# Performance work log

Measured on AMD Instinct MI355X. Metric: run time of the kernel, lower is better.

## Reference

```python
import jax, jax.numpy as jnp
import numpy as np
from functools import partial

NUM_ITERS = 3
NUM_CAPS = 8      # primary capsule count
NUM_CLASSES = 10
OUT_CH = 16       # digit capsule dim
INPUT_SIZE = 32 * 6 * 6  # 1152 primary capsule units per capsule map


def squash(s, axis=-1):
    # faithful to non_linear_squashing: s * (||s||^2/(1+||s||^2)) / (||s||+1e-10)
    norm_sqr = jnp.sum(s * s, axis=axis, keepdims=True)
    scale = jnp.sqrt(norm_sqr) + 1e-10
    mag = norm_sqr / (1.0 + norm_sqr)
    return s * mag / scale


def conv2d(x, w, b, stride):
    y = jax.lax.conv_general_dilated(
        x, w, window_strides=(stride, stride), padding='VALID',
        dimension_numbers=('NCHW', 'OIHW', 'NCHW'))
    return y + b[None, :, None, None]


def setup_inputs() -> dict:
    key = jax.random.key(0)
    ks = jax.random.split(key, 6)
    B = 256
    x = jax.random.normal(ks[0], (B, 1, 28, 28), dtype=jnp.float32)
    conv_w = jax.random.normal(ks[1], (256, 1, 9, 9), dtype=jnp.float32) * 0.05
    conv_b = jax.random.normal(ks[2], (256,), dtype=jnp.float32) * 0.05
    # 8 primary capsule conv units (256->32 each) fused into one 256->256 conv
    prim_w = jax.random.normal(ks[3], (NUM_CAPS * 32, 256, 9, 9), dtype=jnp.float32) * 0.02
    prim_b = jax.random.normal(ks[4], (NUM_CAPS * 32,), dtype=jnp.float32) * 0.02
    # digit routing weights (input_size, num_classes, out_channels, num_capsules)
    digit_w = jax.random.normal(ks[5], (INPUT_SIZE, NUM_CLASSES, OUT_CH, NUM_CAPS), dtype=jnp.float32)
    return {'x': x, 'conv_w': conv_w, 'conv_b': conv_b,
            'prim_w': prim_w, 'prim_b': prim_b, 'digit_w': digit_w}


def reference(x, conv_w, conv_b, prim_w, prim_b, digit_w):
    B = x.shape[0]
    # conv stack: 1->256 k9 s1 + ReLU  (28 -> 20); pool is MaxPool2d(1,1) = identity
    h = jax.nn.relu(conv2d(x, conv_w, conv_b, stride=1))  # (B,256,20,20)
    # primary capsules: 8 convs 256->32 k9 s2, no activation (nl_activation=False)
    p = conv2d(h, prim_w, prim_b, stride=2)               # (B,256,6,6)
    u = p.reshape(B, NUM_CAPS, -1)                        # (B,8,1152)
    u = squash(u, axis=-1)
    # digit layer with dynamic routing
    # u_i: (B, IS, 8);  u_j_i[b,i,c,o] = sum_k W[i,c,o,k] * u_i[b,i,k]
    u_i = jnp.transpose(u, (0, 2, 1))                     # (B,1152,8)
    u_j_i = jnp.einsum('icok,bik->bico', digit_w, u_i)    # (B,1152,10,16)
    b_ij = jnp.zeros((INPUT_SIZE, NUM_CLASSES), dtype=x.dtype)
    out = None
    for _ in range(NUM_ITERS):
        c_ij = jax.nn.softmax(b_ij, axis=0)               # softmax over input capsules (dim=1 in torch)
        s_j = jnp.einsum('ic,bico->bco', c_ij, u_j_i)     # (B,10,16)
        # original squashes (B,1,C,16,1) along dim=2 == the CLASS axis
        out = squash(s_j, axis=1)                         # (B,10,16)
        # agreement: mean over batch of <u_j_i, v_j>
        u_v = jnp.einsum('bico,bco->ic', u_j_i, out) / B  # (1152,10)
        b_ij = b_ij + u_v
    # torch returns out.squeeze(1) with shape (B, C, 16, 1)
    return out[..., None]
```

## Files before the change

### kernel.cpp

```cpp
#include <hip/hip_runtime.h>
#include <cstdint>
#include <cstddef>


typedef __attribute__((ext_vector_type(8))) short short8;
typedef __attribute__((ext_vector_type(4))) float f32x4;

#define PHALF 2359296

__device__ __forceinline__ unsigned short f2bf_rn(float x) {
    unsigned u = __float_as_uint(x);
    unsigned r = (u + 0x7fffu + ((u >> 16) & 1u)) >> 16;
    return (unsigned short)r;
}

__global__ void k_prep(const float* __restrict__ w2, const float* __restrict__ cw,
                       const float* __restrict__ dw,
                       unsigned short* __restrict__ wt,
                       unsigned short* __restrict__ wb1,
                       float* __restrict__ dwT2) {
    __shared__ float lw[20736];
    int blk = blockIdx.x, t = threadIdx.x;
    if (blk < 256) {
        int ocg = blk >> 3, icg = blk & 7;
        for (int idx = t; idx < 20736; idx += 256) {
            int row = idx / 81, k = idx % 81;
            int oc_l = row >> 5, ic_l = row & 31;
            lw[idx] = w2[((size_t)(ocg * 8 + oc_l) * 256 + icg * 32 + ic_l) * 81 + k];
        }
        __syncthreads();
        for (int idx = t; idx < 2592; idx += 256) {
            int k = idx >> 5;
            int r = idx & 31;
            int oc_l = r >> 2, sl = r & 3;
            unsigned short hi8[8];
            #pragma unroll
            for (int j = 0; j < 8; j++)
                hi8[j] = f2bf_rn(lw[(oc_l * 32 + sl * 8 + j) * 81 + k]);
            size_t o = ((size_t)(k * 256 + ocg * 8 + oc_l)) * 256 + icg * 32 + sl * 8;
            *(uint4*)&wt[o] = *(uint4*)hi8;
        }
    } else if (blk == 256) {
        for (int idx = t; idx < 24576; idx += 256) {
            int j = idx & 7, lane = (idx >> 3) & 63;
            int q = (idx >> 9) % 3, nt = idx / 1536;
            int oc = nt * 16 + (lane & 15);
            int kg = q * 32 + (lane >> 4) * 8 + j;
            float v = (kg < 81) ? cw[oc * 81 + kg] : 0.f;
            wb1[idx] = f2bf_rn(v);
        }
    } else {
        int co = blk - 257;
        int c = co >> 4, o = co & 15;
        const float* base = dw + c * 128 + o * 8;
        float* out = dwT2 + (size_t)co * 9216;
        for (int idx = t; idx < 9216; idx += 256) {
            int i = idx >> 3, k = idx & 7;
            out[idx] = base[(size_t)i * 1280 + k];
        }
    }
}

__global__ __launch_bounds__(256) void k_conv1m(
    const float* __restrict__ x, const unsigned short* __restrict__ wb1,
    const float* __restrict__ cb, unsigned short* __restrict__ h)
{
    __shared__ unsigned short xb[900];
    int b = blockIdx.x, ng = blockIdx.y, t = threadIdx.x;
    int w = t >> 6, l = t & 63;
    for (int idx = t; idx < 900; idx += 256) {
        int row = idx / 30, col = idx % 30;
        float v = (row < 28 && col < 28) ? x[(size_t)b * 784 + row * 28 + col] : 0.f;
        xb[idx] = f2bf_rn(v);
    }
    __syncthreads();
    int lane16 = l & 15, l4 = l >> 4;
    int ntile = (w == 0) ? 7 : 6;
    short8 afr[7][3];
    for (int i = 0; i < 7; i++) {
        if (i < ntile) {
            int mt = w + 4 * i;
            int pix = mt * 16 + lane16;
            int py = pix / 20, px = pix % 20;
            #pragma unroll
            for (int qq = 0; qq < 3; qq++) {
                int kbase = qq * 32 + l4 * 8;
                unsigned short tmp[8];
                int ky = kbase / 9, kx = kbase - 9 * (kbase / 9);
                #pragma unroll
                for (int j = 0; j < 8; j++) {
                    tmp[j] = xb[(py + ky) * 30 + px + kx];
                    kx++; if (kx == 9) { kx = 0; ky++; }
                }
                afr[i][qq] = *(short8*)tmp;
            }
        }
    }
    for (int nt0 = 0; nt0 < 8; nt0++) {
        int nt = ng * 8 + nt0;
        short8 bfr[3];
        #pragma unroll
        for (int qq = 0; qq < 3; qq++)
            bfr[qq] = *(const short8*)&wb1[(nt * 3 + qq) * 512 + l * 8];
        float bias = cb[nt * 16 + lane16];
        f32x4 acc[7] = {};
        for (int i = 0; i < 7; i++) {
            if (i < ntile) {
                #pragma unroll
                for (int qq = 0; qq < 3; qq++)
                    acc[i] = __builtin_amdgcn_mfma_f32_16x16x32_bf16(afr[i][qq], bfr[qq], acc[i], 0, 0, 0);
            }
        }
        for (int i = 0; i < 7; i++) {
            if (i < ntile) {
                int mt = w + 4 * i;
                int pixb = mt * 16 + l4 * 4;
                size_t base = ((size_t)b * 400 + pixb) * 256 + nt * 16 + lane16;
                #pragma unroll
                for (int r = 0; r < 4; r++) {
                    float v = fmaxf(acc[i][r] + bias, 0.f);
                    h[base + (size_t)r * 256] = f2bf_rn(v);
                }
            }
        }
    }
}

__global__ __launch_bounds__(256) void k_conv2m(
    const unsigned short* __restrict__ h,
    const unsigned short* __restrict__ wt,
    float* __restrict__ pp)
{
    __shared__ unsigned short smem[24576];
    const int t = threadIdx.x;
    const int w = t >> 6, l = t & 63;
    const int mb = blockIdx.x, nb = blockIdx.y, z = blockIdx.z;

    const unsigned short* src;
    int nld, sbase;
    unsigned rowbase[16];
    if (w < 2) {
        src = h; nld = 16; sbase = w * 8192;
        #pragma unroll
        for (int ld = 0; ld < 16; ld++) {
            int row = ld * 8 + (l >> 3);
            int c = l & 7;
            int g = c ^ (row & 7);
            int P = mb * 128 + row;
            int b = P / 36, o = P % 36;
            int oy = o / 6, ox = o % 6;
            rowbase[ld] = (unsigned)((b * 400 + oy * 40 + ox * 2) * 256 + z * 128 + w * 64 + g * 8);
        }
    } else {
        int hh = w - 2;
        src = wt; nld = 8; sbase = 16384 + hh * 4096;
        #pragma unroll
        for (int ld = 0; ld < 8; ld++) {
            int oc = ld * 8 + (l >> 3);
            int c = l & 7;
            int g = c ^ (oc & 7);
            rowbase[ld] = (unsigned)((nb * 64 + oc) * 256 + z * 128 + hh * 64 + g * 8);
        }
    }

    const int wm = w & 1, wn = w >> 1;
    const int lane16 = l & 15, q = l >> 4;

    f32x4 acc[4][2] = {};

    for (int ky = 0; ky < 9; ky++) {
        for (int kx = 0; kx < 9; kx++) {
            const unsigned kofs = (w < 2) ? (unsigned)((ky * 20 + kx) * 256)
                                          : (unsigned)((ky * 9 + kx) * 65536);
            __syncthreads();
            for (int ld = 0; ld < nld; ld++) {
                __builtin_amdgcn_global_load_lds(
                    (const __attribute__((address_space(1))) unsigned int*)(const void*)(src + rowbase[ld] + kofs),
                    (__attribute__((address_space(3))) unsigned int*)(void*)(smem + sbase + ld * 512),
                    16, 0, 0);
            }
            __syncthreads();
            #pragma unroll
            for (int hh = 0; hh < 2; hh++) {
                #pragma unroll
                for (int ic2 = 0; ic2 < 2; ic2++) {
                    short8 a[4], b[2];
                    #pragma unroll
                    for (int mt = 0; mt < 4; mt++) {
                        int pixL = wm * 64 + mt * 16 + lane16;
                        int ps = (ic2 * 4 + q) ^ (pixL & 7);
                        a[mt] = *(const short8*)(smem + hh * 8192 + pixL * 64 + ps * 8);
                    }
                    #pragma unroll
                    for (int nt = 0; nt < 2; nt++) {
                        int ocL = wn * 32 + nt * 16 + lane16;
                        int ps = (ic2 * 4 + q) ^ (ocL & 7);
                        b[nt] = *(const short8*)(smem + 16384 + hh * 4096 + ocL * 64 + ps * 8);
                    }
                    #pragma unroll
                    for (int mt = 0; mt < 4; mt++)
                        #pragma unroll
                        for (int nt = 0; nt < 2; nt++)
                            acc[mt][nt] = __builtin_amdgcn_mfma_f32_16x16x32_bf16(a[mt], b[nt], acc[mt][nt], 0, 0, 0);
                }
            }
        }
    }

    float* pout = pp + (size_t)z * PHALF;
    #pragma unroll
    for (int mt = 0; mt < 4; mt++) {
        int pixG = mb * 128 + wm * 64 + mt * 16 + q * 4;
        int b = pixG / 36, p36 = pixG % 36;
        #pragma unroll
        for (int nt = 0; nt < 2; nt++) {
            int oc = nb * 64 + wn * 32 + nt * 16 + lane16;
            f32x4 v = acc[mt][nt];
            *(f32x4*)&pout[((size_t)(b * 256 + oc)) * 36 + p36] = v;
        }
    }
}

__global__ void k_squash1(const float* __restrict__ pp, const float* __restrict__ prim_b,
                          float* __restrict__ U) {
    __shared__ float red[4];
    int b = blockIdx.x >> 3, cap = blockIdx.x & 7;
    int t = threadIdx.x;
    const float* pa = pp + ((size_t)b * 256 + cap * 32) * 36;
    const float* pc = pa + PHALF;
    float v[5];
    float ss = 0.f;
    #pragma unroll
    for (int j = 0; j < 5; j++) {
        int idx = t + j * 256;
        if (idx < 1152) {
            int ch_l = idx / 36;
            float val = pa[idx] + pc[idx] + prim_b[cap * 32 + ch_l];
            v[j] = val; ss += val * val;
        } else v[j] = 0.f;
    }
    for (int off = 32; off; off >>= 1) ss += __shfl_down(ss, off);
    if ((t & 63) == 0) red[t >> 6] = ss;
    __syncthreads();
    float n2 = red[0] + red[1] + red[2] + red[3];
    float f = (n2 / (1.0f + n2)) / (sqrtf(n2) + 1e-10f);
    #pragma unroll
    for (int j = 0; j < 5; j++) {
        int idx = t + j * 256;
        if (idx < 1152) U[(size_t)b * 9216 + idx * 8 + cap] = v[j] * f;
    }
}

__global__ void k_ut(const float* __restrict__ U, float* __restrict__ UT) {
    __shared__ float tl[64][65];
    int ikb = blockIdx.x, bb = blockIdx.y, t = threadIdx.x;
    for (int idx = t; idx < 1024; idx += 256) {
        int row = idx >> 4, c4 = idx & 15;
        float4 v = *(const float4*)&U[(size_t)(bb * 64 + row) * 9216 + ikb * 64 + c4 * 4];
        tl[c4 * 4 + 0][row] = v.x;
        tl[c4 * 4 + 1][row] = v.y;
        tl[c4 * 4 + 2][row] = v.z;
        tl[c4 * 4 + 3][row] = v.w;
    }
    __syncthreads();
    for (int idx = t; idx < 1024; idx += 256) {
        int row = idx >> 4, c4 = idx & 15;
        float4 v = make_float4(tl[row][c4 * 4 + 0], tl[row][c4 * 4 + 1],
                               tl[row][c4 * 4 + 2], tl[row][c4 * 4 + 3]);
        *(float4*)&UT[(size_t)(ikb * 64 + row) * 256 + bb * 64 + c4 * 4] = v;
    }
}

__global__ __launch_bounds__(256) void k_gemm1(const float* __restrict__ U,
                                               const float* __restrict__ dwT2,
                                               const float* __restrict__ bij,
                                               float* __restrict__ part,
                                               int uniform) {
    __shared__ float Us[32 * 36];
    __shared__ float WsT[5120];
    __shared__ float cl[360];
    __shared__ float red[256];
    __shared__ float cmx[10], cinv[10];
    int mb = blockIdx.x, kc = blockIdx.y, t = threadIdx.x;
    int tc = t & 15, tb = t >> 4;

    if (!uniform) {
        int c = t % 10, g = t / 10;
        float lmx = -1e30f;
        if (t < 250)
            for (int i = g; i < 1152; i += 25) lmx = fmaxf(lmx, bij[i * 10 + c]);
        red[t] = lmx;
        __syncthreads();
        if (t < 10) {
            float m = -1e30f;
            #pragma unroll
            for (int g2 = 0; g2 < 25; g2++) m = fmaxf(m, red[g2 * 10 + t]);
            cmx[t] = m;
        }
        __syncthreads();
        float lsum = 0.f;
        if (t < 250) {
            float m = cmx[c];
            for (int i = g; i < 1152; i += 25) lsum += expf(bij[i * 10 + c] - m);
        }
        red[t] = lsum;
        __syncthreads();
        if (t < 10) {
            float s2 = 0.f;
            #pragma unroll
            for (int g2 = 0; g2 < 25; g2++) s2 += red[g2 * 10 + t];
            cinv[t] = 1.0f / s2;
        }
        __syncthreads();
        for (int idx = t; idx < 360; idx += 256) {
            int i = kc * 36 + idx / 10, c2 = idx % 10;
            cl[idx] = expf(bij[i * 10 + c2] - cmx[c2]) * cinv[c2];
        }
    }

    const float uscale = 1.0f / 1152.0f;
    float acc[2][10] = {};
    for (int ks = 0; ks < 9; ks++) {
        __syncthreads();
        {
            int bb = t >> 3, k4 = t & 7;
            *(float4*)&Us[bb * 36 + k4 * 4] =
                *(const float4*)&U[(size_t)(mb * 32 + bb) * 9216 + kc * 288 + ks * 32 + k4 * 4];
        }
        #pragma unroll
        for (int pass = 0; pass < 5; pass++) {
            int s = t + pass * 256;
            int co = s >> 3, p = s & 7;
            int kq = p ^ (co & 7);
            int ikl = ks * 32 + kq * 4;
            float4 v = *(const float4*)&dwT2[(size_t)co * 9216 + kc * 288 + ikl];
            float sc = uniform ? uscale : cl[(ikl >> 3) * 10 + (co >> 4)];
            v.x *= sc; v.y *= sc; v.z *= sc; v.w *= sc;
            *(float4*)&WsT[s * 4] = v;
        }
        __syncthreads();
        float a0[32], a1[32];
        #pragma unroll
        for (int kq = 0; kq < 8; kq++) {
            float4 v0 = *(const float4*)&Us[(tb * 2) * 36 + kq * 4];
            float4 v1 = *(const float4*)&Us[(tb * 2 + 1) * 36 + kq * 4];
            a0[kq * 4 + 0] = v0.x; a0[kq * 4 + 1] = v0.y; a0[kq * 4 + 2] = v0.z; a0[kq * 4 + 3] = v0.w;
            a1[kq * 4 + 0] = v1.x; a1[kq * 4 + 1] = v1.y; a1[kq * 4 + 2] = v1.z; a1[kq * 4 + 3] = v1.w;
        }
        #pragma unroll
        for (int j = 0; j < 10; j++) {
            int co = tc + 16 * j;
            int cx = co & 7, cbase = co * 32;
            #pragma unroll
            for (int kq = 0; kq < 8; kq++) {
                float4 wv = *(const float4*)&WsT[cbase + ((kq ^ cx) << 2)];
                acc[0][j] += a0[kq * 4 + 0] * wv.x; acc[0][j] += a0[kq * 4 + 1] * wv.y;
                acc[0][j] += a0[kq * 4 + 2] * wv.z; acc[0][j] += a0[kq * 4 + 3] * wv.w;
                acc[1][j] += a1[kq * 4 + 0] * wv.x; acc[1][j] += a1[kq * 4 + 1] * wv.y;
                acc[1][j] += a1[kq * 4 + 2] * wv.z; acc[1][j] += a1[kq * 4 + 3] * wv.w;
            }
        }
    }
    #pragma unroll
    for (int r = 0; r < 2; r++)
        #pragma unroll
        for (int j = 0; j < 10; j++)
            part[(size_t)kc * 40960 + (mb * 32 + tb * 2 + r) * 160 + tc + 16 * j] = acc[r][j];
}

__global__ void k_redsq(const float* __restrict__ part, float* __restrict__ outT,
                        float* __restrict__ dout, int last) {
    __shared__ float sl[160];
    __shared__ float n2s[16];
    int b = blockIdx.x, t = threadIdx.x;
    float s = 0.f;
    if (t < 160) {
        for (int kc = 0; kc < 32; kc++) s += part[(size_t)kc * 40960 + b * 160 + t];
        sl[t] = s;
    }
    __syncthreads();
    if (t < 16) {
        float n2 = 0.f;
        #pragma unroll
        for (int c = 0; c < 10; c++) { float v = sl[c * 16 + t]; n2 += v * v; }
        n2s[t] = n2;
    }
    __syncthreads();
    if (t < 160) {
        float n2 = n2s[t & 15];
        float f = (n2 / (1.0f + n2)) / (sqrtf(n2) + 1e-10f);
        float r = s * f;
        if (last) dout[(size_t)b * 160 + t] = r;
        else      outT[(size_t)t * 256 + b] = r;
    }
}

__global__ __launch_bounds__(256) void k_g2uv(const float* __restrict__ UT,
                                              const float* __restrict__ outTg,
                                              const float* __restrict__ dw,
                                              float* __restrict__ bij, int init) {
    __shared__ float UsT[1024];
    __shared__ float OsT[5120];
    __shared__ float dwl[5120];
    __shared__ float sb[320];
    int blk = blockIdx.x, t = threadIdx.x;
    int tc = t & 15, tm = t >> 4;
    for (int idx = t; idx < 5120; idx += 256)
        dwl[idx] = dw[(size_t)blk * 5120 + idx];
    float acc[2][10] = {};
    for (int bs = 0; bs < 256; bs += 32) {
        __syncthreads();
        {
            int m = t >> 3, p = t & 7;
            int kq = p ^ (m & 7);
            *(float4*)&UsT[t * 4] =
                *(const float4*)&UT[(size_t)(blk * 32 + m) * 256 + bs + kq * 4];
        }
        #pragma unroll
        for (int pass = 0; pass < 5; pass++) {
            int s = t + pass * 256;
            int co = s >> 3, p = s & 7;
            int kq = p ^ (co & 7);
            *(float4*)&OsT[s * 4] =
                *(const float4*)&outTg[(size_t)co * 256 + bs + kq * 4];
        }
        __syncthreads();
        float a0[32], a1[32];
        int m0 = tm * 2, m1 = tm * 2 + 1;
        #pragma unroll
        for (int kq = 0; kq < 8; kq++) {
            float4 v0 = *(const float4*)&UsT[m0 * 32 + ((kq ^ (m0 & 7)) << 2)];
            float4 v1 = *(const float4*)&UsT[m1 * 32 + ((kq ^ (m1 & 7)) << 2)];
            a0[kq * 4 + 0] = v0.x; a0[kq * 4 + 1] = v0.y; a0[kq * 4 + 2] = v0.z; a0[kq * 4 + 3] = v0.w;
            a1[kq * 4 + 0] = v1.x; a1[kq * 4 + 1] = v1.y; a1[kq * 4 + 2] = v1.z; a1[kq * 4 + 3] = v1.w;
        }
        #pragma unroll
        for (int j = 0; j < 10; j++) {
            int co = tc + 16 * j;
            int cx = co & 7, cbase = co * 32;
            #pragma unroll
            for (int kq = 0; kq < 8; kq++) {
                float4 wv = *(const float4*)&OsT[cbase + ((kq ^ cx) << 2)];
                acc[0][j] += a0[kq * 4 + 0] * wv.x; acc[0][j] += a0[kq * 4 + 1] * wv.y;
                acc[0][j] += a0[kq * 4 + 2] * wv.z; acc[0][j] += a0[kq * 4 + 3] * wv.w;
                acc[1][j] += a1[kq * 4 + 0] * wv.x; acc[1][j] += a1[kq * 4 + 1] * wv.y;
                acc[1][j] += a1[kq * 4 + 2] * wv.z; acc[1][j] += a1[kq * 4 + 3] * wv.w;
            }
        }
    }
    #pragma unroll
    for (int r = 0; r < 2; r++) {
        int ik_l = tm * 2 + r;
        int i_l = ik_l >> 3, k = ik_l & 7;
        #pragma unroll
        for (int j = 0; j < 10; j++) {
            float v = acc[r][j] * dwl[i_l * 1280 + (j * 16 + tc) * 8 + k];
            v += __shfl_down(v, 8, 16);
            v += __shfl_down(v, 4, 16);
            v += __shfl_down(v, 2, 16);
            v += __shfl_down(v, 1, 16);
            if (tc == 0) sb[ik_l * 10 + j] = v;
        }
    }
    __syncthreads();
    if (t < 40) {
        int i_l = t / 10, c = t % 10;
        float s = 0.f;
        #pragma unroll
        for (int kk = 0; kk < 8; kk++) s += sb[(i_l * 8 + kk) * 10 + c];
        size_t o = (size_t)(blk * 4 + i_l) * 10 + c;
        float val = s * (1.0f / 256.0f);
        if (init) bij[o] = val;
        else      bij[o] += val;
    }
}

extern "C" void kernel_launch(void* const* d_in, const int* in_sizes, int n_in,
                              void* d_out, int out_size, void* d_ws, size_t ws_size,
                              hipStream_t stream) {
    const float* x      = (const float*)d_in[0];
    const float* conv_w = (const float*)d_in[1];
    const float* conv_b = (const float*)d_in[2];
    const float* prim_w = (const float*)d_in[3];
    const float* prim_b = (const float*)d_in[4];
    const float* dw     = (const float*)d_in[5];

    char* wsb = (char*)d_ws;
    unsigned short* h   = (unsigned short*)(wsb);
    unsigned short* wt  = (unsigned short*)(wsb + 52428800);
    float* pp   = (float*)(wsb + 63045632);
    float* U    = (float*)(wsb + 81920000);
    float* dwT2 = (float*)(wsb + 91357184);
    float* part = (float*)(wsb + 97255424);
    float* bij  = (float*)(wsb + 102544384);
    float* outT = (float*)(wsb + 102590464);
    float* UT   = (float*)(wsb + 102754304);
    unsigned short* wb1 = (unsigned short*)(wsb + 112191488);
    float* dout = (float*)d_out;

    k_prep<<<417, 256, 0, stream>>>(prim_w, conv_w, dw, wt, wb1, dwT2);
    k_conv1m<<<dim3(256, 2), 256, 0, stream>>>(x, wb1, conv_b, h);
    k_conv2m<<<dim3(72, 4, 2), 256, 0, stream>>>(h, wt, pp);
    k_squash1<<<2048, 256, 0, stream>>>(pp, prim_b, U);
    k_ut<<<dim3(144, 4), 256, 0, stream>>>(U, UT);

    k_gemm1<<<dim3(8, 32), 256, 0, stream>>>(U, dwT2, bij, part, 1);
    k_redsq<<<256, 256, 0, stream>>>(part, outT, dout, 0);
    k_g2uv<<<288, 256, 0, stream>>>(UT, outT, dw, bij, 1);
    k_gemm1<<<dim3(8, 32), 256, 0, stream>>>(U, dwT2, bij, part, 0);
    k_redsq<<<256, 256, 0, stream>>>(part, outT, dout, 0);
    k_g2uv<<<288, 256, 0, stream>>>(UT, outT, dw, bij, 0);
    k_gemm1<<<dim3(8, 32), 256, 0, stream>>>(U, dwT2, bij, part, 0);
    k_redsq<<<256, 256, 0, stream>>>(part, outT, dout, 1);
}
```

Before: 520.0 us.

## Fuse squash and routing iterations into one persistent kernel with grid barriers

Replaces ten separate launches (squash, transpose, three gemm/reduce/agreement rounds) with a single persistent kernel of 256 blocks that steps through the phases using a global atomic-counter barrier. It also drops the UT transpose by transposing U into shared memory inside the agreement phase. This is meant to remove kernel launch gaps and the extra transpose pass. In exchange it depends on all 256 blocks being co-resident, and the agreement phase over 288 units leaves blocks 32..255 idle while a few blocks do a second unit.

```diff
diff --git a/kernel.cpp b/kernel.cpp
--- a/kernel.cpp
+++ b/kernel.cpp
@@ -221,257 +221,262 @@
     }
 }
 
-__global__ void k_squash1(const float* __restrict__ pp, const float* __restrict__ prim_b,
-                          float* __restrict__ U) {
-    __shared__ float red[4];
-    int b = blockIdx.x >> 3, cap = blockIdx.x & 7;
-    int t = threadIdx.x;
-    const float* pa = pp + ((size_t)b * 256 + cap * 32) * 36;
-    const float* pc = pa + PHALF;
-    float v[5];
-    float ss = 0.f;
-    #pragma unroll
-    for (int j = 0; j < 5; j++) {
-        int idx = t + j * 256;
-        if (idx < 1152) {
-            int ch_l = idx / 36;
-            float val = pa[idx] + pc[idx] + prim_b[cap * 32 + ch_l];
-            v[j] = val; ss += val * val;
-        } else v[j] = 0.f;
-    }
-    for (int off = 32; off; off >>= 1) ss += __shfl_down(ss, off);
-    if ((t & 63) == 0) red[t >> 6] = ss;
+__device__ __forceinline__ void gbar(unsigned* cnt, unsigned target) {
     __syncthreads();
-    float n2 = red[0] + red[1] + red[2] + red[3];
-    float f = (n2 / (1.0f + n2)) / (sqrtf(n2) + 1e-10f);
-    #pragma unroll
-    for (int j = 0; j < 5; j++) {
-        int idx = t + j * 256;
-        if (idx < 1152) U[(size_t)b * 9216 + idx * 8 + cap] = v[j] * f;
-    }
-}
-
-__global__ void k_ut(const float* __restrict__ U, float* __restrict__ UT) {
-    __shared__ float tl[64][65];
-    int ikb = blockIdx.x, bb = blockIdx.y, t = threadIdx.x;
-    for (int idx = t; idx < 1024; idx += 256) {
-        int row = idx >> 4, c4 = idx & 15;
-        float4 v = *(const float4*)&U[(size_t)(bb * 64 + row) * 9216 + ikb * 64 + c4 * 4];
-        tl[c4 * 4 + 0][row] = v.x;
-        tl[c4 * 4 + 1][row] = v.y;
-        tl[c4 * 4 + 2][row] = v.z;
-        tl[c4 * 4 + 3][row] = v.w;
+    if (threadIdx.x == 0) {
+        __threadfence();
+        atomicAdd(cnt, 1u);
+        while (__hip_atomic_load(cnt, __ATOMIC_RELAXED, __HIP_MEMORY_SCOPE_AGENT) < target)
+            __builtin_amdgcn_s_sleep(4);
+        __threadfence();
     }
     __syncthreads();
-    for (int idx = t; idx < 1024; idx += 256) {
-        int row = idx >> 4, c4 = idx & 15;
-        float4 v = make_float4(tl[row][c4 * 4 + 0], tl[row][c4 * 4 + 1],
-                               tl[row][c4 * 4 + 2], tl[row][c4 * 4 + 3]);
-        *(float4*)&UT[(size_t)(ikb * 64 + row) * 256 + bb * 64 + c4 * 4] = v;
-    }
-}
-
-__global__ __launch_bounds__(256) void k_gemm1(const float* __restrict__ U,
-                                               const float* __restrict__ dwT2,
-                                               const float* __restrict__ bij,
-                                               float* __restrict__ part,
-                                               int uniform) {
-    __shared__ float Us[32 * 36];
-    __shared__ float WsT[5120];
-    __shared__ float cl[360];
-    __shared__ float red[256];
-    __shared__ float cmx[10], cinv[10];
-    int mb = blockIdx.x, kc = blockIdx.y, t = threadIdx.x;
-    int tc = t & 15, tb = t >> 4;
-
-    if (!uniform) {
-        int c = t % 10, g = t / 10;
-        float lmx = -1e30f;
-        if (t < 250)
-            for (int i = g; i < 1152; i += 25) lmx = fmaxf(lmx, bij[i * 10 + c]);
-        red[t] = lmx;
+}
+
+__global__ __launch_bounds__(256) void k_route(
+    const float* __restrict__ pp, const float* __restrict__ prim_b,
+    float* __restrict__ U, const float* __restrict__ dwT2,
+    const float* __restrict__ dw,
+    float* __restrict__ part, float* __restrict__ outT,
+    float* __restrict__ bij, float* __restrict__ dout,
+    unsigned* __restrict__ ctr)
+{
+    __shared__ __align__(16) float smem[11712];
+    const int bid = blockIdx.x, t = threadIdx.x;
+    const int tc = t & 15, tb = t >> 4;
+    unsigned tgt = 0;
+
+    for (int u = bid; u < 2048; u += 256) {
         __syncthreads();
-        if (t < 10) {
-            float m = -1e30f;
+        float* red = smem;
+        int b = u >> 3, cap = u & 7;
+        const float* pa = pp + ((size_t)b * 256 + cap * 32) * 36;
+        const float* pc = pa + PHALF;
+        float v[5];
+        float ss = 0.f;
+        #pragma unroll
+        for (int j = 0; j < 5; j++) {
+            int idx = t + j * 256;
+            if (idx < 1152) {
+                int ch_l = idx / 36;
+                float val = pa[idx] + pc[idx] + prim_b[cap * 32 + ch_l];
+                v[j] = val; ss += val * val;
+            } else v[j] = 0.f;
+        }
+        for (int off = 32; off; off >>= 1) ss += __shfl_down(ss, off);
+        if ((t & 63) == 0) red[t >> 6] = ss;
+        __syncthreads();
+        float n2 = red[0] + red[1] + red[2] + red[3];
+        float f = (n2 / (1.0f + n2)) / (sqrtf(n2) + 1e-10f);
+        #pragma unroll
+        for (int j = 0; j < 5; j++) {
+            int idx = t + j * 256;
+            if (idx < 1152) U[(size_t)b * 9216 + idx * 8 + cap] = v[j] * f;
+        }
+    }
+    tgt += 256; gbar(ctr, tgt);
+
+    for (int iter = 0; iter < 3; iter++) {
+        {
+            float* Us   = smem;
+            float* WsT  = smem + 1152;
+            float* cl   = smem + 6272;
+            float* red  = smem + 6632;
+            float* cmx  = smem + 6888;
+            float* cinv = smem + 6898;
+            int mb = bid & 7, kc = bid >> 3;
+
+            if (iter > 0) {
+                int c = t % 10, g = t / 10;
+                float lmx = -1e30f;
+                if (t < 250)
+                    for (int i = g; i < 1152; i += 25) lmx = fmaxf(lmx, bij[i * 10 + c]);
+                red[t] = lmx;
+                __syncthreads();
+                if (t < 10) {
+                    float m = -1e30f;
+                    #pragma unroll
+                    for (int g2 = 0; g2 < 25; g2++) m = fmaxf(m, red[g2 * 10 + t]);
+                    cmx[t] = m;
+                }
+                __syncthreads();
+                float lsum = 0.f;
+                if (t < 250) {
+                    float m = cmx[c];
+                    for (int i = g; i < 1152; i += 25) lsum += expf(bij[i * 10 + c] - m);
+                }
+                red[t] = lsum;
+                __syncthreads();
+                if (t < 10) {
+                    float s2 = 0.f;
+                    #pragma unroll
+                    for (int g2 = 0; g2 < 25; g2++) s2 += red[g2 * 10 + t];
+                    cinv[t] = 1.0f / s2;
+                }
+                __syncthreads();
+                for (int idx = t; idx < 360; idx += 256) {
+                    int i = kc * 36 + idx / 10, c2 = idx % 10;
+                    cl[idx] = expf(bij[i * 10 + c2] - cmx[c2]) * cinv[c2];
+                }
+            }
+
+            const float uscale = 1.0f / 1152.0f;
+            float acc[2][10] = {};
+            for (int ks = 0; ks < 9; ks++) {
+                __syncthreads();
+                {
+                    int bb = t >> 3, k4 = t & 7;
+                    *(float4*)&Us[bb * 36 + k4 * 4] =
+                        *(const float4*)&U[(size_t)(mb * 32 + bb) * 9216 + kc * 288 + ks * 32 + k4 * 4];
+                }
+                #pragma unroll
+                for (int pass = 0; pass < 5; pass++) {
+                    int s = t + pass * 256;
+                    int co = s >> 3, p = s & 7;
+                    int kq = p ^ (co & 7);
+                    int ikl = ks * 32 + kq * 4;
+                    float4 v = *(const float4*)&dwT2[(size_t)co * 9216 + kc * 288 + ikl];
+                    float sc = (iter == 0) ? uscale : cl[(ikl >> 3) * 10 + (co >> 4)];
+                    v.x *= sc; v.y *= sc; v.z *= sc; v.w *= sc;
+                    *(float4*)&WsT[s * 4] = v;
+                }
+                __syncthreads();
+                float a0[32], a1[32];
+                #pragma unroll
+                for (int kq = 0; kq < 8; kq++) {
+                    float4 v0 = *(const float4*)&Us[(tb * 2) * 36 + kq * 4];
+                    float4 v1 = *(const float4*)&Us[(tb * 2 + 1) * 36 + kq * 4];
+                    a0[kq * 4 + 0] = v0.x; a0[kq * 4 + 1] = v0.y; a0[kq * 4 + 2] = v0.z; a0[kq * 4 + 3] = v0.w;
+                    a1[kq * 4 + 0] = v1.x; a1[kq * 4 + 1] = v1.y; a1[kq * 4 + 2] = v1.z; a1[kq * 4 + 3] = v1.w;
+                }
+                #pragma unroll
+                for (int j = 0; j < 10; j++) {
+                    int co = tc + 16 * j;
+                    int cx = co & 7, cbase = co * 32;
+                    #pragma unroll
+                    for (int kq = 0; kq < 8; kq++) {
+                        float4 wv = *(const float4*)&WsT[cbase + ((kq ^ cx) << 2)];
+                        acc[0][j] += a0[kq * 4 + 0] * wv.x; acc[0][j] += a0[kq * 4 + 1] * wv.y;
+                        acc[0][j] += a0[kq * 4 + 2] * wv.z; acc[0][j] += a0[kq * 4 + 3] * wv.w;
+                        acc[1][j] += a1[kq * 4 + 0] * wv.x; acc[1][j] += a1[kq * 4 + 1] * wv.y;
+                        acc[1][j] += a1[kq * 4 + 2] * wv.z; acc[1][j] += a1[kq * 4 + 3] * wv.w;
+                    }
+                }
+            }
             #pragma unroll
-            for (int g2 = 0; g2 < 25; g2++) m = fmaxf(m, red[g2 * 10 + t]);
-            cmx[t] = m;
-        }
-        __syncthreads();
-        float lsum = 0.f;
-        if (t < 250) {
-            float m = cmx[c];
-            for (int i = g; i < 1152; i += 25) lsum += expf(bij[i * 10 + c] - m);
-        }
-        red[t] = lsum;
-        __syncthreads();
-        if (t < 10) {
-            float s2 = 0.f;
+            for (int r = 0; r < 2; r++)
+                #pragma unroll
+                for (int j = 0; j < 10; j++)
+                    part[(size_t)kc * 40960 + (mb * 32 + tb * 2 + r) * 160 + tc + 16 * j] = acc[r][j];
+        }
+        tgt += 256; gbar(ctr, tgt);
+
+        {
+            float* sl  = smem;
+            float* n2s = smem + 160;
+            int b = bid;
+            float s = 0.f;
+            if (t < 160) {
+                for (int kc = 0; kc < 32; kc++) s += part[(size_t)kc * 40960 + b * 160 + t];
+                sl[t] = s;
+            }
+            __syncthreads();
+            if (t < 16) {
+                float n2 = 0.f;
+                #pragma unroll
+                for (int c = 0; c < 10; c++) { float v = sl[c * 16 + t]; n2 += v * v; }
+                n2s[t] = n2;
+            }
+            __syncthreads();
+            if (t < 160) {
+                float n2 = n2s[t & 15];
+                float f = (n2 / (1.0f + n2)) / (sqrtf(n2) + 1e-10f);
+                float r = s * f;
+                if (iter < 2) outT[(size_t)t * 256 + b] = r;
+                else          dout[(size_t)b * 160 + t] = r;
+            }
+        }
+        if (iter == 2) break;
+        tgt += 256; gbar(ctr, tgt);
+
+        for (int u = bid; u < 288; u += 256) {
+            float* UsT = smem;
+            float* OsT = smem + 1152;
+            float* dwl = smem + 6272;
+            float* sb  = smem + 11392;
+            __syncthreads();
+            for (int idx = t; idx < 5120; idx += 256)
+                dwl[idx] = dw[(size_t)u * 5120 + idx];
+            float acc[2][10] = {};
+            for (int bs = 0; bs < 256; bs += 32) {
+                __syncthreads();
+                {
+                    int bb = t >> 3, m4 = t & 7;
+                    float4 v = *(const float4*)&U[(size_t)(bs + bb) * 9216 + u * 32 + m4 * 4];
+                    UsT[(m4 * 4 + 0) * 36 + bb] = v.x;
+                    UsT[(m4 * 4 + 1) * 36 + bb] = v.y;
+                    UsT[(m4 * 4 + 2) * 36 + bb] = v.z;
+                    UsT[(m4 * 4 + 3) * 36 + bb] = v.w;
+                }
+                #pragma unroll
+                for (int pass = 0; pass < 5; pass++) {
+                    int s = t + pass * 256;
+                    int co = s >> 3, p = s & 7;
+                    int kq = p ^ (co & 7);
+                    *(float4*)&OsT[s * 4] =
+                        *(const float4*)&outT[(size_t)co * 256 + bs + kq * 4];
+                }
+                __syncthreads();
+                float a0[32], a1[32];
+                int m0 = tb * 2, m1 = tb * 2 + 1;
+                #pragma unroll
+                for (int kq = 0; kq < 8; kq++) {
+                    float4 v0 = *(const float4*)&UsT[m0 * 36 + kq * 4];
+                    float4 v1 = *(const float4*)&UsT[m1 * 36 + kq * 4];
+                    a0[kq * 4 + 0] = v0.x; a0[kq * 4 + 1] = v0.y; a0[kq * 4 + 2] = v0.z; a0[kq * 4 + 3] = v0.w;
+                    a1[kq * 4 + 0] = v1.x; a1[kq * 4 + 1] = v1.y; a1[kq * 4 + 2] = v1.z; a1[kq * 4 + 3] = v1.w;
+                }
+                #pragma unroll
+                for (int j = 0; j < 10; j++) {
+                    int co = tc + 16 * j;
+                    int cx = co & 7, cbase = co * 32;
+                    #pragma unroll
+                    for (int kq = 0; kq < 8; kq++) {
+                        float4 wv = *(const float4*)&OsT[cbase + ((kq ^ cx) << 2)];
+                        acc[0][j] += a0[kq * 4 + 0] * wv.x; acc[0][j] += a0[kq * 4 + 1] * wv.y;
+                        acc[0][j] += a0[kq * 4 + 2] * wv.z; acc[0][j] += a0[kq * 4 + 3] * wv.w;
+                        acc[1][j] += a1[kq * 4 + 0] * wv.x; acc[1][j] += a1[kq * 4 + 1] * wv.y;
+                        acc[1][j] += a1[kq * 4 + 2] * wv.z; acc[1][j] += a1[kq * 4 + 3] * wv.w;
+                    }
+                }
+            }
             #pragma unroll
-            for (int g2 = 0; g2 < 25; g2++) s2 += red[g2 * 10 + t];
-            cinv[t] = 1.0f / s2;
-        }
-        __syncthreads();
-        for (int idx = t; idx < 360; idx += 256) {
-            int i = kc * 36 + idx / 10, c2 = idx % 10;
-            cl[idx] = expf(bij[i * 10 + c2] - cmx[c2]) * cinv[c2];
-        }
-    }
-
-    const float uscale = 1.0f / 1152.0f;
-    float acc[2][10] = {};
-    for (int ks = 0; ks < 9; ks++) {
-        __syncthreads();
-        {
-            int bb = t >> 3, k4 = t & 7;
-            *(float4*)&Us[bb * 36 + k4 * 4] =
-                *(const float4*)&U[(size_t)(mb * 32 + bb) * 9216 + kc * 288 + ks * 32 + k4 * 4];
-        }
-        #pragma unroll
-        for (int pass = 0; pass < 5; pass++) {
-            int s = t + pass * 256;
-            int co = s >> 3, p = s & 7;
-            int kq = p ^ (co & 7);
-            int ikl = ks * 32 + kq * 4;
-            float4 v = *(const float4*)&dwT2[(size_t)co * 9216 + kc * 288 + ikl];
-            float sc = uniform ? uscale : cl[(ikl >> 3) * 10 + (co >> 4)];
-            v.x *= sc; v.y *= sc; v.z *= sc; v.w *= sc;
-            *(float4*)&WsT[s * 4] = v;
-        }
-        __syncthreads();
-        float a0[32], a1[32];
-        #pragma unroll
-        for (int kq = 0; kq < 8; kq++) {
-            float4 v0 = *(const float4*)&Us[(tb * 2) * 36 + kq * 4];
-            float4 v1 = *(const float4*)&Us[(tb * 2 + 1) * 36 + kq * 4];
-            a0[kq * 4 + 0] = v0.x; a0[kq * 4 + 1] = v0.y; a0[kq * 4 + 2] = v0.z; a0[kq * 4 + 3] = v0.w;
-            a1[kq * 4 + 0] = v1.x; a1[kq * 4 + 1] = v1.y; a1[kq * 4 + 2] = v1.z; a1[kq * 4 + 3] = v1.w;
-        }
-        #pragma unroll
-        for (int j = 0; j < 10; j++) {
-            int co = tc + 16 * j;
-            int cx = co & 7, cbase = co * 32;
-            #pragma unroll
-            for (int kq = 0; kq < 8; kq++) {
-                float4 wv = *(const float4*)&WsT[cbase + ((kq ^ cx) << 2)];
-                acc[0][j] += a0[kq * 4 + 0] * wv.x; acc[0][j] += a0[kq * 4 + 1] * wv.y;
-                acc[0][j] += a0[kq * 4 + 2] * wv.z; acc[0][j] += a0[kq * 4 + 3] * wv.w;
-                acc[1][j] += a1[kq * 4 + 0] * wv.x; acc[1][j] += a1[kq * 4 + 1] * wv.y;
-                acc[1][j] += a1[kq * 4 + 2] * wv.z; acc[1][j] += a1[kq * 4 + 3] * wv.w;
-            }
-        }
-    }
-    #pragma unroll
-    for (int r = 0; r < 2; r++)
-        #pragma unroll
-        for (int j = 0; j < 10; j++)
-            part[(size_t)kc * 40960 + (mb * 32 + tb * 2 + r) * 160 + tc + 16 * j] = acc[r][j];
-}
-
-__global__ void k_redsq(const float* __restrict__ part, float* __restrict__ outT,
-                        float* __restrict__ dout, int last) {
-    __shared__ float sl[160];
-    __shared__ float n2s[16];
-    int b = blockIdx.x, t = threadIdx.x;
-    float s = 0.f;
-    if (t < 160) {
-        for (int kc = 0; kc < 32; kc++) s += part[(size_t)kc * 40960 + b * 160 + t];
-        sl[t] = s;
-    }
-    __syncthreads();
-    if (t < 16) {
-        float n2 = 0.f;
-        #pragma unroll
-        for (int c = 0; c < 10; c++) { float v = sl[c * 16 + t]; n2 += v * v; }
-        n2s[t] = n2;
-    }
-    __syncthreads();
-    if (t < 160) {
-        float n2 = n2s[t & 15];
-        float f = (n2 / (1.0f + n2)) / (sqrtf(n2) + 1e-10f);
-        float r = s * f;
-        if (last) dout[(size_t)b * 160 + t] = r;
-        else      outT[(size_t)t * 256 + b] = r;
-    }
-}
-
-__global__ __launch_bounds__(256) void k_g2uv(const float* __restrict__ UT,
-                                              const float* __restrict__ outTg,
-                                              const float* __restrict__ dw,
-                                              float* __restrict__ bij, int init) {
-    __shared__ float UsT[1024];
-    __shared__ float OsT[5120];
-    __shared__ float dwl[5120];
-    __shared__ float sb[320];
-    int blk = blockIdx.x, t = threadIdx.x;
-    int tc = t & 15, tm = t >> 4;
-    for (int idx = t; idx < 5120; idx += 256)
-        dwl[idx] = dw[(size_t)blk * 5120 + idx];
-    float acc[2][10] = {};
-    for (int bs = 0; bs < 256; bs += 32) {
-        __syncthreads();
-        {
-            int m = t >> 3, p = t & 7;
-            int kq = p ^ (m & 7);
-            *(float4*)&UsT[t * 4] =
-                *(const float4*)&UT[(size_t)(blk * 32 + m) * 256 + bs + kq * 4];
-        }
-        #pragma unroll
-        for (int pass = 0; pass < 5; pass++) {
-            int s = t + pass * 256;
-            int co = s >> 3, p = s & 7;
-            int kq = p ^ (co & 7);
-            *(float4*)&OsT[s * 4] =
-                *(const float4*)&outTg[(size_t)co * 256 + bs + kq * 4];
-        }
-        __syncthreads();
-        float a0[32], a1[32];
-        int m0 = tm * 2, m1 = tm * 2 + 1;
-        #pragma unroll
-        for (int kq = 0; kq < 8; kq++) {
-            float4 v0 = *(const float4*)&UsT[m0 * 32 + ((kq ^ (m0 & 7)) << 2)];
-            float4 v1 = *(const float4*)&UsT[m1 * 32 + ((kq ^ (m1 & 7)) << 2)];
-            a0[kq * 4 + 0] = v0.x; a0[kq * 4 + 1] = v0.y; a0[kq * 4 + 2] = v0.z; a0[kq * 4 + 3] = v0.w;
-            a1[kq * 4 + 0] = v1.x; a1[kq * 4 + 1] = v1.y; a1[kq * 4 + 2] = v1.z; a1[kq * 4 + 3] = v1.w;
-        }
-        #pragma unroll
-        for (int j = 0; j < 10; j++) {
-            int co = tc + 16 * j;
-            int cx = co & 7, cbase = co * 32;
-            #pragma unroll
-            for (int kq = 0; kq < 8; kq++) {
-                float4 wv = *(const float4*)&OsT[cbase + ((kq ^ cx) << 2)];
-                acc[0][j] += a0[kq * 4 + 0] * wv.x; acc[0][j] += a0[kq * 4 + 1] * wv.y;
-                acc[0][j] += a0[kq * 4 + 2] * wv.z; acc[0][j] += a0[kq * 4 + 3] * wv.w;
-                acc[1][j] += a1[kq * 4 + 0] * wv.x; acc[1][j] += a1[kq * 4 + 1] * wv.y;
-                acc[1][j] += a1[kq * 4 + 2] * wv.z; acc[1][j] += a1[kq * 4 + 3] * wv.w;
-            }
-        }
-    }
-    #pragma unroll
-    for (int r = 0; r < 2; r++) {
-        int ik_l = tm * 2 + r;
-        int i_l = ik_l >> 3, k = ik_l & 7;
-        #pragma unroll
-        for (int j = 0; j < 10; j++) {
-            float v = acc[r][j] * dwl[i_l * 1280 + (j * 16 + tc) * 8 + k];
-            v += __shfl_down(v, 8, 16);
-            v += __shfl_down(v, 4, 16);
-            v += __shfl_down(v, 2, 16);
-            v += __shfl_down(v, 1, 16);
-            if (tc == 0) sb[ik_l * 10 + j] = v;
-        }
-    }
-    __syncthreads();
-    if (t < 40) {
-        int i_l = t / 10, c = t % 10;
-        float s = 0.f;
-        #pragma unroll
-        for (int kk = 0; kk < 8; kk++) s += sb[(i_l * 8 + kk) * 10 + c];
-        size_t o = (size_t)(blk * 4 + i_l) * 10 + c;
-        float val = s * (1.0f / 256.0f);
-        if (init) bij[o] = val;
-        else      bij[o] += val;
+            for (int r = 0; r < 2; r++) {
+                int ik_l = tb * 2 + r;
+                int i_l = ik_l >> 3, k = ik_l & 7;
+                #pragma unroll
+                for (int j = 0; j < 10; j++) {
+                    float v = acc[r][j] * dwl[i_l * 1280 + (j * 16 + tc) * 8 + k];
+                    v += __shfl_down(v, 8, 16);
+                    v += __shfl_down(v, 4, 16);
+                    v += __shfl_down(v, 2, 16);
+                    v += __shfl_down(v, 1, 16);
+                    if (tc == 0) sb[ik_l * 10 + j] = v;
+                }
+            }
+            __syncthreads();
+            if (t < 40) {
+                int i_l = t / 10, c = t % 10;
+                float s = 0.f;
+                #pragma unroll
+                for (int kk = 0; kk < 8; kk++) s += sb[(i_l * 8 + kk) * 10 + c];
+                size_t o = (size_t)(u * 4 + i_l) * 10 + c;
+                float val = s * (1.0f / 256.0f);
+                if (iter == 0) bij[o] = val;
+                else           bij[o] += val;
+            }
+        }
+        tgt += 256; gbar(ctr, tgt);
     }
 }
 
@@ -494,22 +499,14 @@
     float* part = (float*)(wsb + 97255424);
     float* bij  = (float*)(wsb + 102544384);
     float* outT = (float*)(wsb + 102590464);
-    float* UT   = (float*)(wsb + 102754304);
     unsigned short* wb1 = (unsigned short*)(wsb + 112191488);
+    unsigned* ctr = (unsigned*)(wsb + 112240640);
     float* dout = (float*)d_out;
 
+    hipMemsetAsync(ctr, 0, 64, stream);
     k_prep<<<417, 256, 0, stream>>>(prim_w, conv_w, dw, wt, wb1, dwT2);
     k_conv1m<<<dim3(256, 2), 256, 0, stream>>>(x, wb1, conv_b, h);
     k_conv2m<<<dim3(72, 4, 2), 256, 0, stream>>>(h, wt, pp);
-    k_squash1<<<2048, 256, 0, stream>>>(pp, prim_b, U);
-    k_ut<<<dim3(144, 4), 256, 0, stream>>>(U, UT);
-
-    k_gemm1<<<dim3(8, 32), 256, 0, stream>>>(U, dwT2, bij, part, 1);
-    k_redsq<<<256, 256, 0, stream>>>(part, outT, dout, 0);
-    k_g2uv<<<288, 256, 0, stream>>>(UT, outT, dw, bij, 1);
-    k_gemm1<<<dim3(8, 32), 256, 0, stream>>>(U, dwT2, bij, part, 0);
-    k_redsq<<<256, 256, 0, stream>>>(part, outT, dout, 0);
-    k_g2uv<<<288, 256, 0, stream>>>(UT, outT, dw, bij, 0);
-    k_gemm1<<<dim3(8, 32), 256, 0, stream>>>(U, dwT2, bij, part, 0);
-    k_redsq<<<256, 256, 0, stream>>>(part, outT, dout, 1);
-}
+    k_route<<<256, 256, 0, stream>>>(pp, prim_b, U, dwT2, dw,
+                                     part, outT, bij, dout, ctr);
+}
```

Measured after the change: 745.7 us. 1.43x slower.
